# Kernel optimization log

Hardware: AMD Instinct MI355X
Metric: run time of the kernel (lower is better)

The kernel has to match this reference:

```python
import jax, jax.numpy as jnp
import numpy as np

B, S, D = 2, 2048, 768
H = 12
HD = D // H


def setup_inputs() -> dict:
    key = jax.random.key(0)
    ks = jax.random.split(key, 9)
    s_in = 1.0 / np.sqrt(D)
    return {
        "x": jax.random.normal(ks[0], (B, S, D), dtype=jnp.float32),
        "wq": jax.random.normal(ks[1], (D, D), dtype=jnp.float32) * s_in,
        "bq": jax.random.normal(ks[2], (D,), dtype=jnp.float32) * 0.01,
        "wk": jax.random.normal(ks[3], (D, D), dtype=jnp.float32) * s_in,
        "bk": jax.random.normal(ks[4], (D,), dtype=jnp.float32) * 0.01,
        "wv": jax.random.normal(ks[5], (D, D), dtype=jnp.float32) * s_in,
        "bv": jax.random.normal(ks[6], (D,), dtype=jnp.float32) * 0.01,
        "wo": jax.random.normal(ks[7], (D, D), dtype=jnp.float32) * s_in,
        "bo": jax.random.normal(ks[8], (D,), dtype=jnp.float32) * 0.01,
    }


def reference(x, wq, bq, wk, bk, wv, bv, wo, bo):
    b, s, _ = x.shape
    # projections -> [b, h, s, hd]
    def proj(w, bias):
        return (x @ w + bias).reshape(b, s, H, HD).transpose(0, 2, 1, 3)
    q = proj(wq, bq)
    k = proj(wk, bk)
    v = proj(wv, bv)
    scores = jnp.einsum("bhqd,bhkd->bhqk", q, k)
    causal = jnp.triu(jnp.ones((s, s), dtype=bool), k=1)
    scores = jnp.where(causal, -jnp.inf, scores)
    attn = jax.nn.softmax(scores / np.sqrt(HD), axis=-1)
    # dropout p=0.0 -> identity
    ctx = jnp.einsum("bhqk,bhkd->bhqd", attn, v)
    ctx = ctx.transpose(0, 2, 1, 3).reshape(b, s, D)
    return ctx @ wo + bo
```

## Files before the change

kernel.cpp:

```cpp
#include <hip/hip_runtime.h>
#include <math.h>

#define BB  2
#define SS  2048
#define DD  768
#define HH  12
#define HDD 64
#define BSR (BB * SS)
#define NQT (SS / 64)
#define NCH 80

typedef __attribute__((ext_vector_type(8))) short bf16x8;
typedef __attribute__((ext_vector_type(4))) float f32x4;
typedef __attribute__((ext_vector_type(4))) int  i32x4;

__device__ inline f32x4 mfma16(bf16x8 a, bf16x8 b, f32x4 c) {
    return __builtin_amdgcn_mfma_f32_16x16x32_bf16(a, b, c, 0, 0, 0);
}

__device__ inline unsigned short f2b(float f) {
    unsigned int u = __float_as_uint(f);
    u += 0x7FFFu + ((u >> 16) & 1u);
    return (unsigned short)(u >> 16);
}
__device__ inline float b2f(unsigned short u) {
    return __uint_as_float((unsigned int)u << 16);
}

__device__ inline void async_copy16(void* lds, const void* g) {
    __builtin_amdgcn_global_load_lds(
        (const __attribute__((address_space(1))) unsigned int*)g,
        (__attribute__((address_space(3))) unsigned int*)lds, 16, 0, 0);
}

__global__ __launch_bounds__(256) void conv_x_kernel(
    const float* __restrict__ x, unsigned short* __restrict__ xb)
{
    int id = blockIdx.x * 256 + threadIdx.x;
    size_t base = (size_t)id * 8;
    float4 a = *(const float4*)&x[base];
    float4 b = *(const float4*)&x[base + 4];
    unsigned short o[8] = {f2b(a.x), f2b(a.y), f2b(a.z), f2b(a.w),
                           f2b(b.x), f2b(b.y), f2b(b.z), f2b(b.w)};
    *(i32x4*)&xb[base] = *(const i32x4*)o;
}

__global__ __launch_bounds__(256) void conv_wT_kernel(
    const float* __restrict__ w0, const float* __restrict__ w1,
    const float* __restrict__ w2, const float* __restrict__ w3,
    unsigned short* __restrict__ o0, unsigned short* __restrict__ o1,
    unsigned short* __restrict__ o2, unsigned short* __restrict__ o3)
{
    const float* w = (blockIdx.z == 0) ? w0 : (blockIdx.z == 1) ? w1
                   : (blockIdx.z == 2) ? w2 : w3;
    unsigned short* o = (blockIdx.z == 0) ? o0 : (blockIdx.z == 1) ? o1
                      : (blockIdx.z == 2) ? o2 : o3;
    const int n0 = blockIdx.x * 64;
    const int k0 = blockIdx.y * 64;
    const int tid = threadIdx.x;

    __shared__ unsigned short tile[64][72];

#pragma unroll
    for (int p = 0; p < 4; ++p) {
        int c  = p * 256 + tid;
        int kr = c >> 4;
        int nc = (c & 15) * 4;
        float4 v = *(const float4*)&w[(size_t)(k0 + kr) * DD + n0 + nc];
        tile[nc + 0][kr] = f2b(v.x);
        tile[nc + 1][kr] = f2b(v.y);
        tile[nc + 2][kr] = f2b(v.z);
        tile[nc + 3][kr] = f2b(v.w);
    }
    __syncthreads();
#pragma unroll
    for (int p = 0; p < 2; ++p) {
        int c  = p * 256 + tid;
        int nr = c >> 3;
        int kc = (c & 7) * 8;
        *(i32x4*)&o[(size_t)(n0 + nr) * DD + k0 + kc] = *(const i32x4*)&tile[nr][kc];
    }
}

__device__ inline void mainloop_64x128(
    const unsigned short* __restrict__ A, const unsigned short* __restrict__ Bt,
    unsigned short (*As)[64], unsigned short (*Bs)[64],
    f32x4 acc[2][4], int m0, int n0, int tid, int mh, int nh, int l16, int quad)
{
    const int swz = l16 & 7;
    for (int k0 = 0; k0 < DD; k0 += 64) {
        __syncthreads();
#pragma unroll
        for (int p = 0; p < 2; ++p) {
            int c  = p * 256 + tid;
            int r  = c >> 3;
            int ch = (c & 7) ^ (r & 7);
            async_copy16(&As[r][(c & 7) * 8], &A[(size_t)(m0 + r) * DD + k0 + ch * 8]);
        }
#pragma unroll
        for (int p = 0; p < 4; ++p) {
            int c  = p * 256 + tid;
            int r  = c >> 3;
            int ch = (c & 7) ^ (r & 7);
            async_copy16(&Bs[r][(c & 7) * 8], &Bt[(size_t)(n0 + r) * DD + k0 + ch * 8]);
        }
        __syncthreads();
        bf16x8 af0[2], af1[2], bf0[4], bf1[4];
#pragma unroll
        for (int mt = 0; mt < 2; ++mt) {
            int r = mh * 32 + mt * 16 + l16;
            af0[mt] = *(const bf16x8*)&As[r][((quad    ) ^ swz) * 8];
            af1[mt] = *(const bf16x8*)&As[r][((quad + 4) ^ swz) * 8];
        }
#pragma unroll
        for (int nt = 0; nt < 4; ++nt) {
            int r = nh * 64 + nt * 16 + l16;
            bf0[nt] = *(const bf16x8*)&Bs[r][((quad    ) ^ swz) * 8];
            bf1[nt] = *(const bf16x8*)&Bs[r][((quad + 4) ^ swz) * 8];
        }
#pragma unroll
        for (int mt = 0; mt < 2; ++mt)
#pragma unroll
            for (int nt = 0; nt < 4; ++nt) {
                acc[mt][nt] = mfma16(af0[mt], bf0[nt], acc[mt][nt]);
                acc[mt][nt] = mfma16(af1[mt], bf1[nt], acc[mt][nt]);
            }
    }
}

__global__ __launch_bounds__(256) void qkv_gemm_kernel(
    const unsigned short* __restrict__ xb,
    const unsigned short* __restrict__ wqT, const unsigned short* __restrict__ wkT,
    const unsigned short* __restrict__ wvT,
    const float* __restrict__ bq, const float* __restrict__ bk,
    const float* __restrict__ bv,
    unsigned short* __restrict__ Qg, unsigned short* __restrict__ Kg,
    unsigned short* __restrict__ Vg)
{
    const int which = blockIdx.z;
    const unsigned short* Bt = (which == 0) ? wqT : (which == 1) ? wkT : wvT;
    const float* bias        = (which == 0) ? bq  : (which == 1) ? bk  : bv;
    unsigned short* out      = (which == 0) ? Qg  : (which == 1) ? Kg  : Vg;
    const float qs           = (which == 0) ? 0.125f : 1.0f;

    const int m0 = blockIdx.x * 64;
    const int n0 = blockIdx.y * 128;
    const int tid  = threadIdx.x;
    const int w    = tid >> 6;
    const int lane = tid & 63;
    const int quad = lane >> 4;
    const int l16  = lane & 15;
    const int mh   = w & 1;
    const int nh   = w >> 1;

    __shared__ unsigned short smem[12288];
    unsigned short (*As)[64]  = (unsigned short(*)[64])smem;
    unsigned short (*Bs)[64]  = (unsigned short(*)[64])(smem + 4096);
    unsigned short (*T)[136]  = (unsigned short(*)[136])smem;

    f32x4 zero = {0.f, 0.f, 0.f, 0.f};
    f32x4 acc[2][4];
#pragma unroll
    for (int i = 0; i < 2; ++i)
#pragma unroll
        for (int j = 0; j < 4; ++j) acc[i][j] = zero;

    mainloop_64x128(xb, Bt, As, Bs, acc, m0, n0, tid, mh, nh, l16, quad);

    __syncthreads();

    if (which < 2) {
#pragma unroll
        for (int nt = 0; nt < 4; ++nt) {
            const int col = nh * 64 + nt * 16 + l16;
            const float bvv = bias[n0 + col];
#pragma unroll
            for (int mt = 0; mt < 2; ++mt)
#pragma unroll
                for (int r = 0; r < 4; ++r)
                    T[mh * 32 + mt * 16 + quad * 4 + r][col] =
                        f2b((acc[mt][nt][r] + bvv) * qs);
        }
        __syncthreads();
#pragma unroll
        for (int p2 = 0; p2 < 4; ++p2) {
            int c    = p2 * 256 + tid;
            int row  = c >> 4;
            int ck   = c & 15;
            int head = ck >> 3;
            int wi   = ck & 7;
            int sg   = m0 + row;
            int bi   = sg >> 11, si = sg & 2047;
            int hcol = (n0 >> 6) + head;
            *(i32x4*)&out[(((size_t)(bi * HH + hcol)) * SS + si) * HDD + wi * 8] =
                *(const i32x4*)&T[row][head * 64 + wi * 8];
        }
    } else {
        for (int pass = 0; pass < 2; ++pass) {
            if (pass) __syncthreads();
            if (nh == pass) {
#pragma unroll
                for (int nt = 0; nt < 4; ++nt) {
                    const float bvv = bias[n0 + pass * 64 + nt * 16 + l16];
#pragma unroll
                    for (int mt = 0; mt < 2; ++mt) {
                        ushort4 pk;
                        pk.x = f2b(acc[mt][nt][0] + bvv);
                        pk.y = f2b(acc[mt][nt][1] + bvv);
                        pk.z = f2b(acc[mt][nt][2] + bvv);
                        pk.w = f2b(acc[mt][nt][3] + bvv);
                        *(ushort4*)&T[nt * 16 + l16][mh * 32 + mt * 16 + quad * 4] = pk;
                    }
                }
            }
            __syncthreads();
            const int bi   = m0 >> 11;
            const int s0   = m0 & 2047;
            const int hcol = (n0 >> 6) + pass;
#pragma unroll
            for (int p2 = 0; p2 < 2; ++p2) {
                int c    = p2 * 256 + tid;
                int drow = c >> 3;
                int wi   = c & 7;
                *(i32x4*)&out[(((size_t)(bi * HH + hcol)) * HDD + drow) * SS + s0 + wi * 8] =
                    *(const i32x4*)&T[drow][wi * 8];
            }
        }
    }
}

__global__ __launch_bounds__(256) void out_gemm_kernel(
    const unsigned short* __restrict__ cb, const unsigned short* __restrict__ woT,
    const float* __restrict__ bo, float* __restrict__ out)
{
    const int m0 = blockIdx.x * 64;
    const int n0 = blockIdx.y * 128;
    const int tid  = threadIdx.x;
    const int w    = tid >> 6;
    const int lane = tid & 63;
    const int quad = lane >> 4;
    const int l16  = lane & 15;
    const int mh   = w & 1;
    const int nh   = w >> 1;

    __shared__ unsigned short As[64][64];
    __shared__ unsigned short Bs[128][64];

    f32x4 zero = {0.f, 0.f, 0.f, 0.f};
    f32x4 acc[2][4];
#pragma unroll
    for (int i = 0; i < 2; ++i)
#pragma unroll
        for (int j = 0; j < 4; ++j) acc[i][j] = zero;

    mainloop_64x128(cb, woT, As, Bs, acc, m0, n0, tid, mh, nh, l16, quad);

#pragma unroll
    for (int nt = 0; nt < 4; ++nt) {
        const int n = n0 + nh * 64 + nt * 16 + l16;
        const float bvv = bo[n];
#pragma unroll
        for (int mt = 0; mt < 2; ++mt) {
            const int mbase = m0 + mh * 32 + mt * 16 + quad * 4;
#pragma unroll
            for (int r = 0; r < 4; ++r)
                out[(size_t)(mbase + r) * DD + n] = acc[mt][nt][r] + bvv;
        }
    }
}

__global__ __launch_bounds__(256, 4) void attn_mfma_kernel(
    const unsigned short* __restrict__ Qg, const unsigned short* __restrict__ Kg,
    const unsigned short* __restrict__ Vg, unsigned short* __restrict__ Opart,
    float* __restrict__ Lb)
{
    const int c = (NCH - 1) - blockIdx.x;
    int qt, ck;
    if (c < 8)       { qt = c;                             ck = 0;     }
    else if (c < 24) { int t = c - 8;  qt = 8  + (t >> 1); ck = t & 1; }
    else if (c < 48) { int t = c - 24; qt = 16 + t / 3;    ck = t % 3; }
    else             { int t = c - 48; qt = 24 + (t >> 2); ck = t & 3; }
    const int lo = ck * 8;
    const int hi = min(lo + 8, qt + 1);

    const int h  = blockIdx.y;
    const int b  = blockIdx.z;
    const int tid  = threadIdx.x;
    const int w    = tid >> 6;
    const int lane = tid & 63;
    const int quad = lane >> 4;
    const int l16  = lane & 15;
    const int q0   = qt * 64;

    const size_t bh = (size_t)(b * HH + h);
    const unsigned short* qp = Qg + bh * SS * HDD;
    const unsigned short* kp = Kg + bh * SS * HDD;
    const unsigned short* vp = Vg + bh * HDD * SS;

    unsigned short* op = Opart + ((size_t)bh * NCH + c) * 64 * HDD;
    float* lp = Lb + ((size_t)bh * NCH + c) * 64;

    const int qlocal = w * 16 + l16;
    const int query  = q0 + qlocal;

    __shared__ unsigned short Ks[64][64];
    __shared__ unsigned short Vt[64][64];
    __shared__ unsigned short PsT[4][16][72];
    unsigned short* slab = &PsT[w][0][0];

    const bf16x8 qb0 = *(const bf16x8*)&qp[(size_t)query * HDD + quad * 8];
    const bf16x8 qb1 = *(const bf16x8*)&qp[(size_t)query * HDD + 32 + quad * 8];

    const int pr  = tid >> 3;
    const int po8 = tid & 7;
    const int fs  = l16 & 7;

    i32x4 kpre[2], vpre[2];
#pragma unroll
    for (int p = 0; p < 2; ++p) {
        int r  = pr + p * 32;
        int gc = (po8 ^ (r & 7)) * 8;
        kpre[p] = *(const i32x4*)&kp[(size_t)(lo * 64 + r) * HDD + gc];
        vpre[p] = *(const i32x4*)&vp[(size_t)r * SS + lo * 64 + gc];
    }

    f32x4 zero = {0.f, 0.f, 0.f, 0.f};
    f32x4 o_acc[4];
    float l_i = 0.f;
#pragma unroll
    for (int i = 0; i < 4; ++i) o_acc[i] = zero;

    for (int kt = lo; kt < hi; ++kt) {
        const int k0 = kt * 64;
        __syncthreads();
#pragma unroll
        for (int p = 0; p < 2; ++p) {
            int r = pr + p * 32;
            *(i32x4*)&Ks[r][po8 * 8] = kpre[p];
            *(i32x4*)&Vt[r][po8 * 8] = vpre[p];
        }
        __syncthreads();

        if (kt + 1 < hi) {
            const int kn = (kt + 1) * 64;
#pragma unroll
            for (int p = 0; p < 2; ++p) {
                int r  = pr + p * 32;
                int gc = (po8 ^ (r & 7)) * 8;
                kpre[p] = *(const i32x4*)&kp[(size_t)(kn + r) * HDD + gc];
                vpre[p] = *(const i32x4*)&vp[(size_t)r * SS + kn + gc];
            }
        }

        f32x4 s_acc[4];
#pragma unroll
        for (int t = 0; t < 4; ++t) {
            const int row = t * 16 + l16;
            bf16x8 klo = *(const bf16x8*)&Ks[row][((quad    ) ^ fs) * 8];
            bf16x8 khi = *(const bf16x8*)&Ks[row][((quad + 4) ^ fs) * 8];
            s_acc[t] = mfma16(klo, qb0, zero);
            s_acc[t] = mfma16(khi, qb1, s_acc[t]);
        }

        float ps[4][4];
#pragma unroll
        for (int t = 0; t < 4; ++t)
#pragma unroll
            for (int r = 0; r < 4; ++r) {
                const int key = k0 + t * 16 + quad * 4 + r;
                float pv = __expf(s_acc[t][r]);
                if (kt == qt && key > query) pv = 0.f;
                ps[t][r] = pv;
                l_i += pv;
            }

#pragma unroll
        for (int t = 0; t < 4; ++t) {
            ushort4 pk;
            pk.x = f2b(ps[t][0]);
            pk.y = f2b(ps[t][1]);
            pk.z = f2b(ps[t][2]);
            pk.w = f2b(ps[t][3]);
            *(ushort4*)&slab[l16 * 72 + t * 16 + quad * 4] = pk;
        }
        bf16x8 pb0 = *(const bf16x8*)&slab[l16 * 72 + quad * 8];
        bf16x8 pb1 = *(const bf16x8*)&slab[l16 * 72 + 32 + quad * 8];

#pragma unroll
        for (int t2 = 0; t2 < 4; ++t2) {
            const int row = t2 * 16 + l16;
            bf16x8 vlo = *(const bf16x8*)&Vt[row][((quad    ) ^ fs) * 8];
            bf16x8 vhi = *(const bf16x8*)&Vt[row][((quad + 4) ^ fs) * 8];
            o_acc[t2] = mfma16(vlo, pb0, o_acc[t2]);
            o_acc[t2] = mfma16(vhi, pb1, o_acc[t2]);
        }
    }

    l_i += __shfl_xor(l_i, 16);
    l_i += __shfl_xor(l_i, 32);
    if (quad == 0) lp[qlocal] = l_i;
#pragma unroll
    for (int t2 = 0; t2 < 4; ++t2) {
        ushort4 pk;
        pk.x = f2b(o_acc[t2][0]);
        pk.y = f2b(o_acc[t2][1]);
        pk.z = f2b(o_acc[t2][2]);
        pk.w = f2b(o_acc[t2][3]);
        *(ushort4*)&slab[l16 * 72 + t2 * 16 + quad * 4] = pk;
    }
#pragma unroll
    for (int p2 = 0; p2 < 2; ++p2) {
        int cc  = p2 * 64 + lane;
        int row = cc >> 3, dc = cc & 7;
        *(i32x4*)&op[(size_t)(w * 16 + row) * HDD + dc * 8] =
            *(const i32x4*)&slab[row * 72 + dc * 8];
    }
}

__global__ __launch_bounds__(256) void merge_kernel(
    const unsigned short* __restrict__ Opart, const float* __restrict__ Lb,
    unsigned short* __restrict__ cb)
{
    const int qt  = blockIdx.x;
    const int bhn = blockIdx.y;
    const int b   = bhn / HH, h = bhn % HH;
    const int tid = threadIdx.x;
    const int row = tid >> 2;
    const int d0  = (tid & 3) * 16;
    const int q   = qt * 64 + row;

    const int nch = (qt < 8) ? 1 : (qt < 16) ? 2 : (qt < 24) ? 3 : 4;
    const int cb0 = (qt < 8) ? qt
                  : (qt < 16) ? (8  + (qt - 8)  * 2)
                  : (qt < 24) ? (24 + (qt - 16) * 3)
                  :             (48 + (qt - 24) * 4);

    float suml = 0.f;
    float accv[16];
#pragma unroll
    for (int i = 0; i < 16; ++i) accv[i] = 0.f;

    for (int ci = 0; ci < nch; ++ci) {
        const size_t base = (size_t)bhn * NCH + cb0 + ci;
        suml += Lb[base * 64 + row];
        const unsigned short* o = Opart + (base * 64 + row) * HDD + d0;
#pragma unroll
        for (int i = 0; i < 16; ++i) accv[i] += b2f(o[i]);
    }
    const float inv = 1.0f / suml;
    unsigned short res[16];
#pragma unroll
    for (int i = 0; i < 16; ++i) res[i] = f2b(accv[i] * inv);
    unsigned short* dst = &cb[((size_t)(b * SS + q)) * DD + h * HDD + d0];
    *(i32x4*)&dst[0] = *(const i32x4*)&res[0];
    *(i32x4*)&dst[8] = *(const i32x4*)&res[8];
}

extern "C" void kernel_launch(void* const* d_in, const int* in_sizes, int n_in,
                              void* d_out, int out_size, void* d_ws, size_t ws_size,
                              hipStream_t stream)
{
    const float* x  = (const float*)d_in[0];
    const float* wq = (const float*)d_in[1];
    const float* bq = (const float*)d_in[2];
    const float* wk = (const float*)d_in[3];
    const float* bk = (const float*)d_in[4];
    const float* wv = (const float*)d_in[5];
    const float* bv = (const float*)d_in[6];
    const float* wo = (const float*)d_in[7];
    const float* bo = (const float*)d_in[8];
    float* out = (float*)d_out;

    char* p = (char*)d_ws;
    const size_t XB  = (size_t)BSR * DD * 2;
    const size_t WB  = (size_t)DD * DD * 2;
    const size_t OPB = (size_t)BB * HH * NCH * 64 * HDD * 2;
    const size_t LBB = (size_t)BB * HH * NCH * 64 * 4;
    unsigned short* xb  = (unsigned short*)p;            p += XB;
    unsigned short* wqT = (unsigned short*)p;            p += WB;
    unsigned short* wkT = (unsigned short*)p;            p += WB;
    unsigned short* wvT = (unsigned short*)p;            p += WB;
    unsigned short* woT = (unsigned short*)p;            p += WB;
    unsigned short* Qg  = (unsigned short*)p;            p += XB;
    unsigned short* Kg  = (unsigned short*)p;            p += XB;
    unsigned short* Vg  = (unsigned short*)p;            p += XB;
    unsigned short* cb  = (unsigned short*)p;            p += XB;
    unsigned short* Opart = (unsigned short*)p;          p += OPB;
    float* Lb = (float*)p;                               p += LBB;

    conv_x_kernel<<<BSR * DD / (256 * 8), 256, 0, stream>>>(x, xb);
    conv_wT_kernel<<<dim3(DD / 64, DD / 64, 4), 256, 0, stream>>>(
        wq, wk, wv, wo, wqT, wkT, wvT, woT);
    qkv_gemm_kernel<<<dim3(BSR / 64, DD / 128, 3), 256, 0, stream>>>(
        xb, wqT, wkT, wvT, bq, bk, bv, Qg, Kg, Vg);
    attn_mfma_kernel<<<dim3(NCH, HH, BB), 256, 0, stream>>>(
        Qg, Kg, Vg, Opart, Lb);
    merge_kernel<<<dim3(NQT, BB * HH), 256, 0, stream>>>(Opart, Lb, cb);
    out_gemm_kernel<<<dim3(BSR / 64, DD / 128), 256, 0, stream>>>(cb, woT, bo, out);
}
```

Baseline: 161.4 us.

## Merge conversion kernels and enlarge QKV GEMM tile to 128x128 with swizzled LDS

The separate x and weight conversion kernels become one launch, with a z-slice of blocks running a grid-stride loop over x. The QKV projection GEMM tile grows from 64x128 to 128x128, with an inline mainloop that uses XOR-swizzled LDS chunks and 16 accumulators per wave. The goal is more operand reuse per loaded tile and one fewer kernel launch. In exchange it uses more registers and LDS, launches half as many GEMM blocks, and needs two-pass epilogues.

```diff
diff --git a/kernel.cpp b/kernel.cpp
--- a/kernel.cpp
+++ b/kernel.cpp
@@ -33,31 +33,31 @@
         (__attribute__((address_space(3))) unsigned int*)lds, 16, 0, 0);
 }
 
-__global__ __launch_bounds__(256) void conv_x_kernel(
-    const float* __restrict__ x, unsigned short* __restrict__ xb)
-{
-    int id = blockIdx.x * 256 + threadIdx.x;
-    size_t base = (size_t)id * 8;
-    float4 a = *(const float4*)&x[base];
-    float4 b = *(const float4*)&x[base + 4];
-    unsigned short o[8] = {f2b(a.x), f2b(a.y), f2b(a.z), f2b(a.w),
-                           f2b(b.x), f2b(b.y), f2b(b.z), f2b(b.w)};
-    *(i32x4*)&xb[base] = *(const i32x4*)o;
-}
-
-__global__ __launch_bounds__(256) void conv_wT_kernel(
+__global__ __launch_bounds__(256) void conv_kernel(
+    const float* __restrict__ x, unsigned short* __restrict__ xb,
     const float* __restrict__ w0, const float* __restrict__ w1,
     const float* __restrict__ w2, const float* __restrict__ w3,
     unsigned short* __restrict__ o0, unsigned short* __restrict__ o1,
     unsigned short* __restrict__ o2, unsigned short* __restrict__ o3)
 {
+    const int tid = threadIdx.x;
+    if (blockIdx.z == 4) {
+        for (int b2 = blockIdx.x; b2 < BSR * DD / (256 * 8); b2 += 144) {
+            size_t base = ((size_t)b2 * 256 + tid) * 8;
+            float4 a = *(const float4*)&x[base];
+            float4 b = *(const float4*)&x[base + 4];
+            unsigned short o[8] = {f2b(a.x), f2b(a.y), f2b(a.z), f2b(a.w),
+                                   f2b(b.x), f2b(b.y), f2b(b.z), f2b(b.w)};
+            *(i32x4*)&xb[base] = *(const i32x4*)o;
+        }
+        return;
+    }
     const float* w = (blockIdx.z == 0) ? w0 : (blockIdx.z == 1) ? w1
                    : (blockIdx.z == 2) ? w2 : w3;
     unsigned short* o = (blockIdx.z == 0) ? o0 : (blockIdx.z == 1) ? o1
                       : (blockIdx.z == 2) ? o2 : o3;
-    const int n0 = blockIdx.x * 64;
-    const int k0 = blockIdx.y * 64;
-    const int tid = threadIdx.x;
+    const int n0 = (blockIdx.x % 12) * 64;
+    const int k0 = (blockIdx.x / 12) * 64;
 
     __shared__ unsigned short tile[64][72];
 
@@ -143,7 +143,7 @@
     unsigned short* out      = (which == 0) ? Qg  : (which == 1) ? Kg  : Vg;
     const float qs           = (which == 0) ? 0.125f : 1.0f;
 
-    const int m0 = blockIdx.x * 64;
+    const int m0 = blockIdx.x * 128;
     const int n0 = blockIdx.y * 128;
     const int tid  = threadIdx.x;
     const int w    = tid >> 6;
@@ -152,48 +152,91 @@
     const int l16  = lane & 15;
     const int mh   = w & 1;
     const int nh   = w >> 1;
-
-    __shared__ unsigned short smem[12288];
+    const int swz  = l16 & 7;
+
+    __shared__ unsigned short smem[16384];
     unsigned short (*As)[64]  = (unsigned short(*)[64])smem;
-    unsigned short (*Bs)[64]  = (unsigned short(*)[64])(smem + 4096);
+    unsigned short (*Bs)[64]  = (unsigned short(*)[64])(smem + 8192);
     unsigned short (*T)[136]  = (unsigned short(*)[136])smem;
 
     f32x4 zero = {0.f, 0.f, 0.f, 0.f};
-    f32x4 acc[2][4];
-#pragma unroll
-    for (int i = 0; i < 2; ++i)
+    f32x4 acc[4][4];
+#pragma unroll
+    for (int i = 0; i < 4; ++i)
 #pragma unroll
         for (int j = 0; j < 4; ++j) acc[i][j] = zero;
 
-    mainloop_64x128(xb, Bt, As, Bs, acc, m0, n0, tid, mh, nh, l16, quad);
+    for (int k0 = 0; k0 < DD; k0 += 64) {
+        __syncthreads();
+#pragma unroll
+        for (int p = 0; p < 4; ++p) {
+            int c  = p * 256 + tid;
+            int r  = c >> 3;
+            int ch = (c & 7) ^ (r & 7);
+            async_copy16(&As[r][(c & 7) * 8], &xb[(size_t)(m0 + r) * DD + k0 + ch * 8]);
+        }
+#pragma unroll
+        for (int p = 0; p < 4; ++p) {
+            int c  = p * 256 + tid;
+            int r  = c >> 3;
+            int ch = (c & 7) ^ (r & 7);
+            async_copy16(&Bs[r][(c & 7) * 8], &Bt[(size_t)(n0 + r) * DD + k0 + ch * 8]);
+        }
+        __syncthreads();
+        bf16x8 af0[4], af1[4], bf0[4], bf1[4];
+#pragma unroll
+        for (int mt = 0; mt < 4; ++mt) {
+            int r = mh * 64 + mt * 16 + l16;
+            af0[mt] = *(const bf16x8*)&As[r][((quad    ) ^ swz) * 8];
+            af1[mt] = *(const bf16x8*)&As[r][((quad + 4) ^ swz) * 8];
+        }
+#pragma unroll
+        for (int nt = 0; nt < 4; ++nt) {
+            int r = nh * 64 + nt * 16 + l16;
+            bf0[nt] = *(const bf16x8*)&Bs[r][((quad    ) ^ swz) * 8];
+            bf1[nt] = *(const bf16x8*)&Bs[r][((quad + 4) ^ swz) * 8];
+        }
+#pragma unroll
+        for (int mt = 0; mt < 4; ++mt)
+#pragma unroll
+            for (int nt = 0; nt < 4; ++nt) {
+                acc[mt][nt] = mfma16(af0[mt], bf0[nt], acc[mt][nt]);
+                acc[mt][nt] = mfma16(af1[mt], bf1[nt], acc[mt][nt]);
+            }
+    }
 
     __syncthreads();
 
     if (which < 2) {
-#pragma unroll
-        for (int nt = 0; nt < 4; ++nt) {
-            const int col = nh * 64 + nt * 16 + l16;
-            const float bvv = bias[n0 + col];
-#pragma unroll
-            for (int mt = 0; mt < 2; ++mt)
-#pragma unroll
-                for (int r = 0; r < 4; ++r)
-                    T[mh * 32 + mt * 16 + quad * 4 + r][col] =
-                        f2b((acc[mt][nt][r] + bvv) * qs);
-        }
-        __syncthreads();
-#pragma unroll
-        for (int p2 = 0; p2 < 4; ++p2) {
-            int c    = p2 * 256 + tid;
-            int row  = c >> 4;
-            int ck   = c & 15;
-            int head = ck >> 3;
-            int wi   = ck & 7;
-            int sg   = m0 + row;
-            int bi   = sg >> 11, si = sg & 2047;
-            int hcol = (n0 >> 6) + head;
-            *(i32x4*)&out[(((size_t)(bi * HH + hcol)) * SS + si) * HDD + wi * 8] =
-                *(const i32x4*)&T[row][head * 64 + wi * 8];
+        for (int pass = 0; pass < 2; ++pass) {
+            if (pass) __syncthreads();
+            if (mh == pass) {
+#pragma unroll
+                for (int nt = 0; nt < 4; ++nt) {
+                    const int col = nh * 64 + nt * 16 + l16;
+                    const float bvv = bias[n0 + col];
+#pragma unroll
+                    for (int mt = 0; mt < 4; ++mt)
+#pragma unroll
+                        for (int r = 0; r < 4; ++r)
+                            T[mt * 16 + quad * 4 + r][col] =
+                                f2b((acc[mt][nt][r] + bvv) * qs);
+                }
+            }
+            __syncthreads();
+#pragma unroll
+            for (int p2 = 0; p2 < 4; ++p2) {
+                int c    = p2 * 256 + tid;
+                int row  = c >> 4;
+                int ck   = c & 15;
+                int head = ck >> 3;
+                int wi   = ck & 7;
+                int sg   = m0 + pass * 64 + row;
+                int bi   = sg >> 11, si = sg & 2047;
+                int hcol = (n0 >> 6) + head;
+                *(i32x4*)&out[(((size_t)(bi * HH + hcol)) * SS + si) * HDD + wi * 8] =
+                    *(const i32x4*)&T[row][head * 64 + wi * 8];
+            }
         }
     } else {
         for (int pass = 0; pass < 2; ++pass) {
@@ -203,13 +246,13 @@
                 for (int nt = 0; nt < 4; ++nt) {
                     const float bvv = bias[n0 + pass * 64 + nt * 16 + l16];
 #pragma unroll
-                    for (int mt = 0; mt < 2; ++mt) {
+                    for (int mt = 0; mt < 4; ++mt) {
                         ushort4 pk;
                         pk.x = f2b(acc[mt][nt][0] + bvv);
                         pk.y = f2b(acc[mt][nt][1] + bvv);
                         pk.z = f2b(acc[mt][nt][2] + bvv);
                         pk.w = f2b(acc[mt][nt][3] + bvv);
-                        *(ushort4*)&T[nt * 16 + l16][mh * 32 + mt * 16 + quad * 4] = pk;
+                        *(ushort4*)&T[nt * 16 + l16][mh * 64 + mt * 16 + quad * 4] = pk;
                     }
                 }
             }
@@ -218,10 +261,10 @@
             const int s0   = m0 & 2047;
             const int hcol = (n0 >> 6) + pass;
 #pragma unroll
-            for (int p2 = 0; p2 < 2; ++p2) {
+            for (int p2 = 0; p2 < 4; ++p2) {
                 int c    = p2 * 256 + tid;
-                int drow = c >> 3;
-                int wi   = c & 7;
+                int drow = c >> 4;
+                int wi   = c & 15;
                 *(i32x4*)&out[(((size_t)(bi * HH + hcol)) * HDD + drow) * SS + s0 + wi * 8] =
                     *(const i32x4*)&T[drow][wi * 8];
             }
@@ -488,10 +531,9 @@
     unsigned short* Opart = (unsigned short*)p;          p += OPB;
     float* Lb = (float*)p;                               p += LBB;
 
-    conv_x_kernel<<<BSR * DD / (256 * 8), 256, 0, stream>>>(x, xb);
-    conv_wT_kernel<<<dim3(DD / 64, DD / 64, 4), 256, 0, stream>>>(
-        wq, wk, wv, wo, wqT, wkT, wvT, woT);
-    qkv_gemm_kernel<<<dim3(BSR / 64, DD / 128, 3), 256, 0, stream>>>(
+    conv_kernel<<<dim3(144, 1, 5), 256, 0, stream>>>(
+        x, xb, wq, wk, wv, wo, wqT, wkT, wvT, woT);
+    qkv_gemm_kernel<<<dim3(BSR / 128, DD / 128, 3), 256, 0, stream>>>(
         xb, wqT, wkT, wvT, bq, bk, bv, Qg, Kg, Vg);
     attn_mfma_kernel<<<dim3(NCH, HH, BB), 256, 0, stream>>>(
         Qg, Kg, Vg, Opart, Lb);
```

Result: slower. 182.5 us (+13.1%).
